# Kernel tuning notes

Measured on AMD Instinct MI355X. Metric: run time of the kernel, lower is better.

Reference implementation:

```python
import jax, jax.numpy as jnp
import numpy as np

N = 4096      # nodes
FEAT = 512    # feature_size
HID = 256     # hidden_dim
E = 131072    # edges (avg degree 32)


def setup_inputs() -> dict:
    key = jax.random.key(0)
    ks = jax.random.split(key, 10)
    x = jax.random.normal(ks[0], (N, FEAT), dtype=jnp.float32)
    edge_index = jax.random.randint(ks[1], (2, E), 0, N)
    edge_attr = jax.random.uniform(ks[2], (E, 1), dtype=jnp.float32)
    # nn.Linear(bias=False) weights, stored as [in, out] so k = x @ Wk
    Wk = jax.random.normal(ks[3], (FEAT, HID), dtype=jnp.float32) / np.sqrt(FEAT)
    Wq = jax.random.normal(ks[4], (FEAT, HID), dtype=jnp.float32) / np.sqrt(FEAT)
    Wv = jax.random.normal(ks[5], (FEAT, FEAT), dtype=jnp.float32) / np.sqrt(FEAT)
    # EmbeddingTable.reset_parameters: normal(0, 1), shape [num_embeddings=2, dim]
    Ek = jax.random.normal(ks[6], (2, HID), dtype=jnp.float32)
    Eq = jax.random.normal(ks[7], (2, HID), dtype=jnp.float32)
    Ev = jax.random.normal(ks[8], (2, FEAT), dtype=jnp.float32)
    # ContinuousEmbeddingIndex params
    idx_bias = jnp.full((1,), 0.5, dtype=jnp.float32)
    idx_mult = jnp.full((1,), 10.0, dtype=jnp.float32)
    return dict(x=x, edge_index=edge_index, edge_attr=edge_attr,
                Wk=Wk, Wq=Wq, Wv=Wv, Ek=Ek, Eq=Eq, Ev=Ev,
                idx_bias=idx_bias, idx_mult=idx_mult)


def reference(x, edge_index, edge_attr, Wk, Wq, Wv, Ek, Eq, Ev, idx_bias, idx_mult):
    n = x.shape[0]
    L = x.shape[-1]  # feature_size, used as softmax scale
    src, dst = edge_index[0], edge_index[1]

    # ContinuousEmbeddingIndex: soft 2-way interpolation weights [E, 2]
    s = jax.nn.sigmoid((edge_attr - idx_bias) * idx_mult)
    w = jnp.concatenate([s, 1.0 - s], axis=-1)

    # per-edge relative embeddings (EmbeddingTable: weights @ embeddings)
    rk = w @ Ek   # [E, HID]
    rq = w @ Eq   # [E, HID]
    rv = w @ Ev   # [E, FEAT]

    k = x @ Wk    # [N, HID]
    q = x @ Wq    # [N, HID]
    v = x @ Wv    # [N, FEAT]

    # A = q k^T + (q_i . Rk_ij) + (k_j . Rq_ij) + q k^T
    # The Rk/Rq terms are nonzero only on edges -> compute per-edge and scatter-add
    # (to_dense_adj sums duplicate edges, matched by .add).
    A = 2.0 * (q @ k.T)                                   # [N, N]
    edge_bias = jnp.sum(q[src] * rk, axis=-1) + jnp.sum(k[dst] * rq, axis=-1)  # [E]
    A = A.at[src, dst].add(edge_bias)
    A = jax.nn.softmax(A / np.sqrt(L), axis=-1)           # dropout = identity (eval)

    # M = A v + sum_j A_ij * Rv_ij  (second term only nonzero on edges)
    M = A @ v
    M = M + jax.ops.segment_sum(A[src, dst][:, None] * rv, src, num_segments=n)
    return M
```

## Files before the change

### kernel.cpp

```cpp
#include <hip/hip_runtime.h>
#include <hip/hip_bf16.h>
#include <cmath>


typedef short bf16x8 __attribute__((ext_vector_type(8)));
typedef float f32x4  __attribute__((ext_vector_type(4)));
typedef unsigned short ushort_t;
typedef unsigned short ushort8v __attribute__((ext_vector_type(8)));

constexpr int BUCKET = 64;

__device__ __forceinline__ ushort_t f2bf(float f) {
    union { float f; unsigned u; } v; v.f = f;
    unsigned u = v.u;
    u += 0x7FFFu + ((u >> 16) & 1u);
    return (ushort_t)(u >> 16);
}
__device__ __forceinline__ float bf2f(ushort_t h) {
    union { unsigned u; float f; } v; v.u = ((unsigned)h) << 16;
    return v.f;
}
__device__ __forceinline__ ushort_t f2h(float f) {
    union { _Float16 h; ushort_t u; } v; v.h = (_Float16)f; return v.u;
}
__device__ __forceinline__ float h2f(ushort_t u) {
    union { ushort_t u; _Float16 h; } v; v.u = u; return (float)v.h;
}
__device__ __forceinline__ void gload_lds16(const void* g, void* l) {
    __builtin_amdgcn_global_load_lds(
        (const __attribute__((address_space(1))) void*)g,
        (__attribute__((address_space(3))) void*)l, 16, 0, 0);
}

__device__ __forceinline__ void gemm_core(
    const ushort_t* __restrict__ A, const ushort_t* __restrict__ B,
    int lda, int ldb, int Ksz, size_t kbase, int bm, int bn,
    ushort_t* As, ushort_t* Bs, f32x4 (&acc)[4][4])
{
    constexpr int BK = 32;
    const int tid  = threadIdx.x;
    const int lane = tid & 63;
    const int wid  = tid >> 6;
    const int wm = (wid >> 1) * 64;
    const int wn = (wid & 1) * 64;

    const int r0 = tid >> 2;
    const int c8 = (tid & 3) * 8;
    const ushort_t* Ag0 = A + (size_t)(bm + r0) * lda + kbase + c8;
    const ushort_t* Bg0 = B + (size_t)(bn + r0) * ldb + kbase + c8;
    const ushort_t* Ag1 = Ag0 + (size_t)64 * lda;
    const ushort_t* Bg1 = Bg0 + (size_t)64 * ldb;
    ushort_t* AsW0 = &As[(wid * 64) * 8];
    ushort_t* AsW1 = &As[(256 + wid * 64) * 8];
    ushort_t* BsW0 = &Bs[(wid * 64) * 8];
    ushort_t* BsW1 = &Bs[(256 + wid * 64) * 8];

    const int fr = lane & 15;
    const int kh = (lane >> 4) * 8;

    for (int k0 = 0; k0 < Ksz; k0 += BK) {
        gload_lds16(Ag0 + k0, AsW0);
        gload_lds16(Ag1 + k0, AsW1);
        gload_lds16(Bg0 + k0, BsW0);
        gload_lds16(Bg1 + k0, BsW1);
        __syncthreads();

        bf16x8 af[4], bfv[4];
        #pragma unroll
        for (int i = 0; i < 4; ++i) {
            af[i]  = *(const bf16x8*)&As[(wm + i * 16 + fr) * 32 + kh];
            bfv[i] = *(const bf16x8*)&Bs[(wn + i * 16 + fr) * 32 + kh];
        }
        #pragma unroll
        for (int i = 0; i < 4; ++i)
            #pragma unroll
            for (int j = 0; j < 4; ++j)
                acc[i][j] = __builtin_amdgcn_mfma_f32_16x16x32_bf16(
                    af[i], bfv[j], acc[i][j], 0, 0, 0);
        __syncthreads();
    }
}

__device__ __forceinline__ int swizzle_bid()
{
    int bid = blockIdx.y * gridDim.x + blockIdx.x;
    const int nwg = gridDim.x * gridDim.y;
    if ((nwg & 7) == 0) {
        const int cpx = nwg >> 3;
        bid = (bid & 7) * cpx + (bid >> 3);
    }
    return bid;
}

template<int MODE>
__global__ __launch_bounds__(256) void gemm_nt_mfma(
    const ushort_t* __restrict__ A, const ushort_t* __restrict__ B,
    void* __restrict__ Cv, int lda, int ldb, int ldc, int Ksz, float alpha)
{
    __shared__ ushort_t As[128 * 32];
    __shared__ ushort_t Bs[128 * 32];
    const int bid = swizzle_bid();
    const int bm = (bid / gridDim.x) * 128;
    const int bn = (bid % gridDim.x) * 128;
    f32x4 acc[4][4] = {};
    gemm_core(A, B, lda, ldb, Ksz, 0, bm, bn, As, Bs, acc);

    const int lane = threadIdx.x & 63;
    const int wid  = threadIdx.x >> 6;
    const int wm = (wid >> 1) * 64, wn = (wid & 1) * 64;
    const int cr = (lane >> 4) * 4, cc = lane & 15;
    #pragma unroll
    for (int i = 0; i < 4; ++i)
        #pragma unroll
        for (int j = 0; j < 4; ++j) {
            const int col = bn + wn + j * 16 + cc;
            const int rowb = bm + wm + i * 16 + cr;
            #pragma unroll
            for (int jj = 0; jj < 4; ++jj) {
                const float val = alpha * acc[i][j][jj];
                if (MODE == 0)
                    ((float*)Cv)[(size_t)(rowb + jj) * ldc + col] = val;
                else if (MODE == 1)
                    ((ushort_t*)Cv)[(size_t)(rowb + jj) * ldc + col] = f2bf(val);
                else
                    ((ushort_t*)Cv)[(size_t)(rowb + jj) * ldc + col] = f2h(val);
            }
        }
}

__global__ __launch_bounds__(256) void proj_gemm(
    const ushort_t* __restrict__ xb, const ushort_t* __restrict__ Wqkt,
    const ushort_t* __restrict__ Wvt, ushort_t* __restrict__ qkb,
    ushort_t* __restrict__ vTb, int FEAT, int HID, int N)
{
    __shared__ ushort_t As[128 * 32];
    __shared__ ushort_t Bs[128 * 32];
    const int b = blockIdx.x;
    const ushort_t* A; const ushort_t* B; ushort_t* C;
    int bm, bn, ldc;
    if (b < 128) {
        const int gx = (2 * HID) / 128;
        bm = (b / gx) * 128; bn = (b % gx) * 128;
        A = xb; B = Wqkt; C = qkb; ldc = 2 * HID;
    } else {
        const int b2 = b - 128;
        const int gx = N / 128;
        bm = (b2 / gx) * 128; bn = (b2 % gx) * 128;
        A = Wvt; B = xb; C = vTb; ldc = N;
    }
    f32x4 acc[4][4] = {};
    gemm_core(A, B, FEAT, FEAT, FEAT, 0, bm, bn, As, Bs, acc);

    const int lane = threadIdx.x & 63;
    const int wid  = threadIdx.x >> 6;
    const int wm = (wid >> 1) * 64, wn = (wid & 1) * 64;
    const int cr = (lane >> 4) * 4, cc = lane & 15;
    #pragma unroll
    for (int i = 0; i < 4; ++i)
        #pragma unroll
        for (int j = 0; j < 4; ++j) {
            const int col = bn + wn + j * 16 + cc;
            const int rowb = bm + wm + i * 16 + cr;
            #pragma unroll
            for (int jj = 0; jj < 4; ++jj)
                C[(size_t)(rowb + jj) * ldc + col] = f2bf(acc[i][j][jj]);
        }
}

__global__ __launch_bounds__(256) void pv_gemm_splitk(
    const ushort_t* __restrict__ P, const ushort_t* __restrict__ vT,
    ushort_t* __restrict__ parts, int N, int FEAT, int Kchunk)
{
    __shared__ ushort_t As[128 * 32];
    __shared__ ushort_t Bs[128 * 32];
    const int bid = swizzle_bid();
    const int bm = (bid / gridDim.x) * 128;
    const int bn = (bid % gridDim.x) * 128;

    f32x4 acc[4][4] = {};
    gemm_core(P, vT, N, N, Kchunk, (size_t)blockIdx.z * Kchunk, bm, bn, As, Bs, acc);

    const int tid = threadIdx.x;
    const int lane = tid & 63;
    const int wid  = tid >> 6;
    const int wm = (wid >> 1) * 64, wn = (wid & 1) * 64;
    const int cr = (lane >> 4) * 4, cc = lane & 15;
    ushort_t* myPart = parts + (size_t)blockIdx.z * N * FEAT;
    #pragma unroll
    for (int i = 0; i < 4; ++i)
        #pragma unroll
        for (int j = 0; j < 4; ++j) {
            const int col = bn + wn + j * 16 + cc;
            const int rowb = bm + wm + i * 16 + cr;
            #pragma unroll
            for (int jj = 0; jj < 4; ++jj)
                myPart[(size_t)(rowb + jj) * FEAT + col] = f2bf(acc[i][j][jj]);
        }
}

__global__ void reduce_add_rv_kernel(
    const ushort_t* __restrict__ parts, float* __restrict__ out,
    const float* __restrict__ c0, const float* __restrict__ c1,
    const float* __restrict__ Ev, int FEAT, size_t zstride, int nz)
{
    const int i8 = blockIdx.x * 256 + threadIdx.x;
    const int F8 = FEAT / 8;
    const int node = i8 / F8;
    const int f0 = (i8 % F8) * 8;
    float s[8] = {};
    for (int z = 0; z < nz; ++z) {
        const ushort8v p = *(const ushort8v*)(parts + (size_t)z * zstride + (size_t)i8 * 8);
        #pragma unroll
        for (int j = 0; j < 8; ++j) s[j] += bf2f(p[j]);
    }
    const float a0 = c0[node], a1 = c1[node];
    float4 o0, o1;
    const float4 e00 = *(const float4*)(Ev + f0);
    const float4 e01 = *(const float4*)(Ev + f0 + 4);
    const float4 e10 = *(const float4*)(Ev + FEAT + f0);
    const float4 e11 = *(const float4*)(Ev + FEAT + f0 + 4);
    o0.x = s[0] + a0 * e00.x + a1 * e10.x;
    o0.y = s[1] + a0 * e00.y + a1 * e10.y;
    o0.z = s[2] + a0 * e00.z + a1 * e10.z;
    o0.w = s[3] + a0 * e00.w + a1 * e10.w;
    o1.x = s[4] + a0 * e01.x + a1 * e11.x;
    o1.y = s[5] + a0 * e01.y + a1 * e11.y;
    o1.z = s[6] + a0 * e01.z + a1 * e11.z;
    o1.w = s[7] + a0 * e01.w + a1 * e11.w;
    float* op = out + (size_t)node * FEAT + f0;
    *(float4*)op = o0;
    *(float4*)(op + 4) = o1;
}

__global__ __launch_bounds__(256) void prep_kernel(
    const float* __restrict__ x, const float* __restrict__ Wq,
    const float* __restrict__ Wk, const float* __restrict__ Wv,
    ushort_t* __restrict__ xb, ushort_t* __restrict__ Wqkt,
    ushort_t* __restrict__ Wvt, int* __restrict__ rowcnt,
    int N, int FEAT, int HID)
{
    const int b = blockIdx.x;
    const int tid = threadIdx.x;
    const int xBlocks = (N * FEAT / 8) / 256;
    const int qkTiles = (FEAT / 32) * (HID / 32);
    const int vTiles  = (FEAT / 32) * (FEAT / 32);
    const int zBase = xBlocks + 2 * qkTiles + vTiles;

    if (b >= zBase) {
        const int i = (b - zBase) * 256 + tid;
        if (i <= N) rowcnt[i] = 0;
        return;
    }
    if (b < xBlocks) {
        const int i = b * 256 + tid;
        const float4 a = ((const float4*)x)[2 * i];
        const float4 c = ((const float4*)x)[2 * i + 1];
        ushort8v o;
        o[0] = f2bf(a.x); o[1] = f2bf(a.y); o[2] = f2bf(a.z); o[3] = f2bf(a.w);
        o[4] = f2bf(c.x); o[5] = f2bf(c.y); o[6] = f2bf(c.z); o[7] = f2bf(c.w);
        ((ushort8v*)xb)[i] = o;
        return;
    }

    __shared__ float tile[32][33];
    int t = b - xBlocks;
    const float* src; ushort_t* dst; int I, O;
    if (t < qkTiles)            { src = Wq; dst = Wqkt;                       I = FEAT; O = HID; }
    else if (t < 2 * qkTiles)   { src = Wk; dst = Wqkt + (size_t)HID * FEAT;  I = FEAT; O = HID; t -= qkTiles; }
    else                        { src = Wv; dst = Wvt;                        I = FEAT; O = FEAT; t -= 2 * qkTiles; }
    const int ot = O / 32;
    const int r0 = (t / ot) * 32;
    const int c0 = (t % ot) * 32;
    const int lr = tid >> 5;
    const int lc = tid & 31;
    #pragma unroll
    for (int rr = 0; rr < 32; rr += 8)
        tile[lr + rr][lc] = src[(size_t)(r0 + lr + rr) * O + c0 + lc];
    __syncthreads();
    #pragma unroll
    for (int rr = 0; rr < 32; rr += 8)
        dst[(size_t)(c0 + lr + rr) * I + r0 + lc] = f2bf(tile[lc][lr + rr]);
}

__global__ __launch_bounds__(256) void node_dots(
    const ushort_t* __restrict__ qk,
    const float* __restrict__ Ek, const float* __restrict__ Eq,
    float* qk0, float* qk1, float* kq0, float* kq1,
    float* c0, float* c1, int HID)
{
    const int node = blockIdx.x;
    const int t = threadIdx.x;
    const ushort_t* row = qk + (size_t)node * (2 * HID);
    const float qv = bf2f(row[t]);
    const float kv = bf2f(row[HID + t]);
    float p0 = qv * Ek[t];
    float p1 = qv * Ek[HID + t];
    float p2 = kv * Eq[t];
    float p3 = kv * Eq[HID + t];
    #pragma unroll
    for (int off = 32; off > 0; off >>= 1) {
        p0 += __shfl_down(p0, off);
        p1 += __shfl_down(p1, off);
        p2 += __shfl_down(p2, off);
        p3 += __shfl_down(p3, off);
    }
    __shared__ float red[4][4];
    if ((t & 63) == 0) {
        const int w = t >> 6;
        red[w][0] = p0; red[w][1] = p1; red[w][2] = p2; red[w][3] = p3;
    }
    __syncthreads();
    if (t == 0) {
        qk0[node] = red[0][0] + red[1][0] + red[2][0] + red[3][0];
        qk1[node] = red[0][1] + red[1][1] + red[2][1] + red[3][1];
        kq0[node] = red[0][2] + red[1][2] + red[2][2] + red[3][2];
        kq1[node] = red[0][3] + red[1][3] + red[2][3] + red[3][3];
        c0[node] = 0.f;
        c1[node] = 0.f;
    }
}

__global__ void scatter_kernel(
    const int* __restrict__ ei, const float* __restrict__ attr,
    const float* __restrict__ qk0, const float* __restrict__ qk1,
    const float* __restrict__ kq0, const float* __restrict__ kq1,
    int* __restrict__ rowcnt, int2* __restrict__ ebuf, int4* __restrict__ oflow,
    int E, int N, float scale,
    const float* __restrict__ ibp, const float* __restrict__ imp)
{
    const int e = blockIdx.x * 256 + threadIdx.x;
    if (e >= E) return;
    const int src = ei[e];
    const int dst = ei[E + e];
    const float s = 1.f / (1.f + __expf(-(attr[e] - ibp[0]) * imp[0]));
    const float bias = (s * qk0[src] + (1.f - s) * qk1[src]
                      + s * kq0[dst] + (1.f - s) * kq1[dst]) * scale;
    const int pos = atomicAdd(&rowcnt[src], 1);
    if (pos < BUCKET) {
        int2 rec; rec.x = dst; rec.y = __float_as_int(bias);
        ebuf[(size_t)src * BUCKET + pos] = rec;
    } else {
        const int oi = atomicAdd(&rowcnt[N], 1);
        int4 rec; rec.x = src; rec.y = dst; rec.z = __float_as_int(bias); rec.w = 0;
        oflow[oi] = rec;
    }
}

__global__ __launch_bounds__(256) void softmax_rows_bf16(
    const ushort_t* __restrict__ Ah, const int* __restrict__ rowcnt,
    const int2* __restrict__ ebuf, const int4* __restrict__ oflow,
    ushort_t* __restrict__ P, int N)
{
    __shared__ float lbias[4096];
    __shared__ float red[4];
    const int r = blockIdx.x;
    const ushort_t* a = Ah + (size_t)r * N;
    ushort_t* p = P + (size_t)r * N;
    const int t = threadIdx.x;

    #pragma unroll
    for (int u = 0; u < 4; ++u)
        *(float4*)&lbias[(u * 256 + t) * 4] = float4{0.f, 0.f, 0.f, 0.f};

    float v[16];
    {
        const ushort8v h0 = ((const ushort8v*)a)[t];
        const ushort8v h1 = ((const ushort8v*)a)[256 + t];
        #pragma unroll
        for (int j = 0; j < 8; ++j) { v[j] = h2f(h0[j]); v[8 + j] = h2f(h1[j]); }
    }
    __syncthreads();

    const int cnt = min(rowcnt[r], BUCKET);
    if (t < cnt) {
        const int2 rec = ebuf[(size_t)r * BUCKET + t];
        atomicAdd(&lbias[rec.x], __int_as_float(rec.y));
    }
    const int ocnt = rowcnt[N];
    for (int j = t; j < ocnt; j += 256) {
        const int4 rec = oflow[j];
        if (rec.x == r) atomicAdd(&lbias[rec.y], __int_as_float(rec.z));
    }
    __syncthreads();

    float mx = -1e30f;
    {
        const int b0 = t * 8, b1 = (256 + t) * 8;
        const float4 l0 = *(const float4*)&lbias[b0];
        const float4 l1 = *(const float4*)&lbias[b0 + 4];
        const float4 l2 = *(const float4*)&lbias[b1];
        const float4 l3 = *(const float4*)&lbias[b1 + 4];
        v[0] += l0.x; v[1] += l0.y; v[2]  += l0.z; v[3]  += l0.w;
        v[4] += l1.x; v[5] += l1.y; v[6]  += l1.z; v[7]  += l1.w;
        v[8] += l2.x; v[9] += l2.y; v[10] += l2.z; v[11] += l2.w;
        v[12] += l3.x; v[13] += l3.y; v[14] += l3.z; v[15] += l3.w;
    }
    #pragma unroll
    for (int j = 0; j < 16; ++j) mx = fmaxf(mx, v[j]);
    #pragma unroll
    for (int off = 32; off > 0; off >>= 1) mx = fmaxf(mx, __shfl_down(mx, off));
    if ((t & 63) == 0) red[t >> 6] = mx;
    __syncthreads();
    const float m = fmaxf(fmaxf(red[0], red[1]), fmaxf(red[2], red[3]));
    __syncthreads();

    float sum = 0.f;
    #pragma unroll
    for (int j = 0; j < 16; ++j) { v[j] = __expf(v[j] - m); sum += v[j]; }
    #pragma unroll
    for (int off = 32; off > 0; off >>= 1) sum += __shfl_down(sum, off);
    if ((t & 63) == 0) red[t >> 6] = sum;
    __syncthreads();
    const float inv = 1.f / (red[0] + red[1] + red[2] + red[3]);

    ushort8v o0, o1;
    #pragma unroll
    for (int j = 0; j < 8; ++j) {
        o0[j] = f2bf(v[j] * inv);
        o1[j] = f2bf(v[8 + j] * inv);
    }
    ((ushort8v*)p)[t] = o0;
    ((ushort8v*)p)[256 + t] = o1;
}

__global__ void edge_coeff_kernel(
    const int* __restrict__ ei, const float* __restrict__ attr,
    const ushort_t* __restrict__ P, float* __restrict__ c0, float* __restrict__ c1,
    int E, int N, const float* __restrict__ ibp, const float* __restrict__ imp)
{
    const int e = blockIdx.x * blockDim.x + threadIdx.x;
    if (e >= E) return;
    const int src = ei[e];
    const int dst = ei[E + e];
    const float s = 1.f / (1.f + __expf(-(attr[e] - ibp[0]) * imp[0]));
    const float pv = bf2f(P[(size_t)src * N + dst]);
    atomicAdd(&c0[src], pv * s);
    atomicAdd(&c1[src], pv * (1.f - s));
}

extern "C" void kernel_launch(void* const* d_in, const int* in_sizes, int n_in,
                              void* d_out, int out_size, void* d_ws, size_t ws_size,
                              hipStream_t stream)
{
    const float* x    = (const float*)d_in[0];
    const int*   ei   = (const int*)d_in[1];
    const float* attr = (const float*)d_in[2];
    const float* Wk   = (const float*)d_in[3];
    const float* Wq   = (const float*)d_in[4];
    const float* Wv   = (const float*)d_in[5];
    const float* Ek   = (const float*)d_in[6];
    const float* Eq   = (const float*)d_in[7];
    const float* Ev   = (const float*)d_in[8];
    const float* ib   = (const float*)d_in[9];
    const float* im   = (const float*)d_in[10];
    float* out = (float*)d_out;

    const int FEAT = (int)lroundf(sqrtf((float)in_sizes[5]));
    const int HID  = in_sizes[3] / FEAT;
    const int N    = in_sizes[0] / FEAT;
    const int E    = in_sizes[2];

    char* w = (char*)d_ws;
    size_t o = 0;
    ushort_t* xb   = (ushort_t*)(w + o); o += (size_t)N * FEAT * 2;
    ushort_t* Wqkt = (ushort_t*)(w + o); o += (size_t)2 * HID * FEAT * 2;
    ushort_t* Wvt  = (ushort_t*)(w + o); o += (size_t)FEAT * FEAT * 2;
    ushort_t* qkb  = (ushort_t*)(w + o); o += (size_t)N * 2 * HID * 2;
    ushort_t* vTb  = (ushort_t*)(w + o); o += (size_t)FEAT * N * 2;
    ushort_t* Ah   = (ushort_t*)(w + o); o += (size_t)N * N * 2;
    ushort_t* Pb   = (ushort_t*)(w + o); o += (size_t)N * N * 2;
    float*    qk0  = (float*)(w + o);    o += (size_t)N * 4;
    float*    qk1  = (float*)(w + o);    o += (size_t)N * 4;
    float*    kq0  = (float*)(w + o);    o += (size_t)N * 4;
    float*    kq1  = (float*)(w + o);    o += (size_t)N * 4;
    float*    c0   = (float*)(w + o);    o += (size_t)N * 4;
    float*    c1   = (float*)(w + o);    o += (size_t)N * 4;
    int*      rowcnt = (int*)(w + o);    o += (size_t)(N + 8) * 4;
    o = (o + 15) & ~(size_t)15;
    int2*     ebuf   = (int2*)(w + o);   o += (size_t)N * BUCKET * 8;
    int4*     oflow  = (int4*)(w + o);   o += (size_t)E * 16;
    ushort_t* pvpart = Ah;

    const dim3 blk(256);
    const int NZ = 4;
    const int Kchunk = N / NZ;
    const float scale = 1.f / sqrtf((float)FEAT);

    const int xBlocks = (N * FEAT / 8) / 256;
    const int qkTiles = (FEAT / 32) * (HID / 32);
    const int vTiles  = (FEAT / 32) * (FEAT / 32);
    const int zBlocks = (N + 1 + 255) / 256;
    prep_kernel<<<xBlocks + 2 * qkTiles + vTiles + zBlocks, blk, 0, stream>>>(
        x, Wq, Wk, Wv, xb, Wqkt, Wvt, rowcnt, N, FEAT, HID);

    proj_gemm<<<256, blk, 0, stream>>>(xb, Wqkt, Wvt, qkb, vTb, FEAT, HID, N);

    node_dots<<<N, blk, 0, stream>>>(qkb, Ek, Eq, qk0, qk1, kq0, kq1, c0, c1, HID);

    scatter_kernel<<<(E + 255) / 256, blk, 0, stream>>>(
        ei, attr, qk0, qk1, kq0, kq1, rowcnt, ebuf, oflow, E, N, scale, ib, im);

    gemm_nt_mfma<2><<<dim3(N / 128, N / 128), blk, 0, stream>>>(
        qkb, qkb + HID, Ah, 2 * HID, 2 * HID, N, HID, 2.f * scale);

    softmax_rows_bf16<<<N, blk, 0, stream>>>(Ah, rowcnt, ebuf, oflow, Pb, N);

    edge_coeff_kernel<<<(E + 255) / 256, blk, 0, stream>>>(ei, attr, Pb, c0, c1, E, N, ib, im);

    pv_gemm_splitk<<<dim3(FEAT / 128, N / 128, NZ), blk, 0, stream>>>(
        Pb, vTb, pvpart, N, FEAT, Kchunk);

    reduce_add_rv_kernel<<<(N * FEAT / 8) / 256, blk, 0, stream>>>(
        pvpart, out, c0, c1, Ev, FEAT, (size_t)N * FEAT, NZ);
}
```

Baseline: 128.5 us.

## Fuse edge coefficient accumulation into softmax kernel using shared-memory probabilities

Removes the separate edge_coeff kernel, which gathered P values from global memory and did global atomics per edge. The softmax kernel now keeps the normalized probabilities in shared memory and sums the per-row edge coefficients with shared-memory atomics. The sigmoid weight is stored in the edge bucket records, so the buckets grow from 8 to 16 bytes. This adds an extra barrier and more scatter write traffic, and it also drops the c0/c1 zeroing from node_dots.

```diff
diff --git a/kernel.cpp b/kernel.cpp
--- a/kernel.cpp
+++ b/kernel.cpp
@@ -285,8 +285,7 @@
 __global__ __launch_bounds__(256) void node_dots(
     const ushort_t* __restrict__ qk,
     const float* __restrict__ Ek, const float* __restrict__ Eq,
-    float* qk0, float* qk1, float* kq0, float* kq1,
-    float* c0, float* c1, int HID)
+    float* qk0, float* qk1, float* kq0, float* kq1, int HID)
 {
     const int node = blockIdx.x;
     const int t = threadIdx.x;
@@ -315,8 +314,6 @@
         qk1[node] = red[0][1] + red[1][1] + red[2][1] + red[3][1];
         kq0[node] = red[0][2] + red[1][2] + red[2][2] + red[3][2];
         kq1[node] = red[0][3] + red[1][3] + red[2][3] + red[3][3];
-        c0[node] = 0.f;
-        c1[node] = 0.f;
     }
 }
 
@@ -324,7 +321,7 @@
     const int* __restrict__ ei, const float* __restrict__ attr,
     const float* __restrict__ qk0, const float* __restrict__ qk1,
     const float* __restrict__ kq0, const float* __restrict__ kq1,
-    int* __restrict__ rowcnt, int2* __restrict__ ebuf, int4* __restrict__ oflow,
+    int* __restrict__ rowcnt, int4* __restrict__ ebuf, int4* __restrict__ oflow,
     int E, int N, float scale,
     const float* __restrict__ ibp, const float* __restrict__ imp)
 {
@@ -337,22 +334,26 @@
                       + s * kq0[dst] + (1.f - s) * kq1[dst]) * scale;
     const int pos = atomicAdd(&rowcnt[src], 1);
     if (pos < BUCKET) {
-        int2 rec; rec.x = dst; rec.y = __float_as_int(bias);
+        int4 rec; rec.x = dst; rec.y = __float_as_int(bias);
+        rec.z = __float_as_int(s); rec.w = 0;
         ebuf[(size_t)src * BUCKET + pos] = rec;
     } else {
         const int oi = atomicAdd(&rowcnt[N], 1);
-        int4 rec; rec.x = src; rec.y = dst; rec.z = __float_as_int(bias); rec.w = 0;
+        int4 rec; rec.x = src; rec.y = dst;
+        rec.z = __float_as_int(bias); rec.w = __float_as_int(s);
         oflow[oi] = rec;
     }
 }
 
 __global__ __launch_bounds__(256) void softmax_rows_bf16(
     const ushort_t* __restrict__ Ah, const int* __restrict__ rowcnt,
-    const int2* __restrict__ ebuf, const int4* __restrict__ oflow,
-    ushort_t* __restrict__ P, int N)
+    const int4* __restrict__ ebuf, const int4* __restrict__ oflow,
+    ushort_t* __restrict__ P, float* __restrict__ c0, float* __restrict__ c1,
+    int N)
 {
     __shared__ float lbias[4096];
     __shared__ float red[4];
+    __shared__ float csum[2];
     const int r = blockIdx.x;
     const ushort_t* a = Ah + (size_t)r * N;
     ushort_t* p = P + (size_t)r * N;
@@ -361,6 +362,7 @@
     #pragma unroll
     for (int u = 0; u < 4; ++u)
         *(float4*)&lbias[(u * 256 + t) * 4] = float4{0.f, 0.f, 0.f, 0.f};
+    if (t < 2) csum[t] = 0.f;
 
     float v[16];
     {
@@ -373,7 +375,7 @@
 
     const int cnt = min(rowcnt[r], BUCKET);
     if (t < cnt) {
-        const int2 rec = ebuf[(size_t)r * BUCKET + t];
+        const int4 rec = ebuf[(size_t)r * BUCKET + t];
         atomicAdd(&lbias[rec.x], __int_as_float(rec.y));
     }
     const int ocnt = rowcnt[N];
@@ -414,28 +416,40 @@
     const float inv = 1.f / (red[0] + red[1] + red[2] + red[3]);
 
     ushort8v o0, o1;
-    #pragma unroll
-    for (int j = 0; j < 8; ++j) {
-        o0[j] = f2bf(v[j] * inv);
-        o1[j] = f2bf(v[8 + j] * inv);
+    {
+        const int b0 = t * 8, b1 = (256 + t) * 8;
+        #pragma unroll
+        for (int j = 0; j < 8; ++j) {
+            const float p0 = v[j] * inv;
+            const float p1 = v[8 + j] * inv;
+            o0[j] = f2bf(p0);
+            o1[j] = f2bf(p1);
+            lbias[b0 + j] = p0;
+            lbias[b1 + j] = p1;
+        }
     }
     ((ushort8v*)p)[t] = o0;
     ((ushort8v*)p)[256 + t] = o1;
-}
-
-__global__ void edge_coeff_kernel(
-    const int* __restrict__ ei, const float* __restrict__ attr,
-    const ushort_t* __restrict__ P, float* __restrict__ c0, float* __restrict__ c1,
-    int E, int N, const float* __restrict__ ibp, const float* __restrict__ imp)
-{
-    const int e = blockIdx.x * blockDim.x + threadIdx.x;
-    if (e >= E) return;
-    const int src = ei[e];
-    const int dst = ei[E + e];
-    const float s = 1.f / (1.f + __expf(-(attr[e] - ibp[0]) * imp[0]));
-    const float pv = bf2f(P[(size_t)src * N + dst]);
-    atomicAdd(&c0[src], pv * s);
-    atomicAdd(&c1[src], pv * (1.f - s));
+    __syncthreads();
+
+    if (t < cnt) {
+        const int4 rec = ebuf[(size_t)r * BUCKET + t];
+        const float s = __int_as_float(rec.z);
+        const float pv = lbias[rec.x];
+        atomicAdd(&csum[0], pv * s);
+        atomicAdd(&csum[1], pv * (1.f - s));
+    }
+    for (int j = t; j < ocnt; j += 256) {
+        const int4 rec = oflow[j];
+        if (rec.x == r) {
+            const float s = __int_as_float(rec.w);
+            const float pv = lbias[rec.y];
+            atomicAdd(&csum[0], pv * s);
+            atomicAdd(&csum[1], pv * (1.f - s));
+        }
+    }
+    __syncthreads();
+    if (t == 0) { c0[r] = csum[0]; c1[r] = csum[1]; }
 }
 
 extern "C" void kernel_launch(void* const* d_in, const int* in_sizes, int n_in,
@@ -477,7 +491,7 @@
     float*    c1   = (float*)(w + o);    o += (size_t)N * 4;
     int*      rowcnt = (int*)(w + o);    o += (size_t)(N + 8) * 4;
     o = (o + 15) & ~(size_t)15;
-    int2*     ebuf   = (int2*)(w + o);   o += (size_t)N * BUCKET * 8;
+    int4*     ebuf   = (int4*)(w + o);   o += (size_t)N * BUCKET * 16;
     int4*     oflow  = (int4*)(w + o);   o += (size_t)E * 16;
     ushort_t* pvpart = Ah;
 
@@ -495,7 +509,7 @@
 
     proj_gemm<<<256, blk, 0, stream>>>(xb, Wqkt, Wvt, qkb, vTb, FEAT, HID, N);
 
-    node_dots<<<N, blk, 0, stream>>>(qkb, Ek, Eq, qk0, qk1, kq0, kq1, c0, c1, HID);
+    node_dots<<<N, blk, 0, stream>>>(qkb, Ek, Eq, qk0, qk1, kq0, kq1, HID);
 
     scatter_kernel<<<(E + 255) / 256, blk, 0, stream>>>(
         ei, attr, qk0, qk1, kq0, kq1, rowcnt, ebuf, oflow, E, N, scale, ib, im);
@@ -503,9 +517,7 @@
     gemm_nt_mfma<2><<<dim3(N / 128, N / 128), blk, 0, stream>>>(
         qkb, qkb + HID, Ah, 2 * HID, 2 * HID, N, HID, 2.f * scale);
 
-    softmax_rows_bf16<<<N, blk, 0, stream>>>(Ah, rowcnt, ebuf, oflow, Pb, N);
-
-    edge_coeff_kernel<<<(E + 255) / 256, blk, 0, stream>>>(ei, attr, Pb, c0, c1, E, N, ib, im);
+    softmax_rows_bf16<<<N, blk, 0, stream>>>(Ah, rowcnt, ebuf, oflow, Pb, c0, c1, N);
 
     pv_gemm_splitk<<<dim3(FEAT / 128, N / 128, NZ), blk, 0, stream>>>(
         Pb, vTb, pvpart, N, FEAT, Kchunk);
```

New measurement: 118.5 us. 7.8% less time.
